# Kernel tuning notes

Hardware: AMD Instinct MI355X
Metric: run time of the kernel (lower is better)

## Reference

```python
import jax, jax.numpy as jnp
import numpy as np

EMBED_DIM = 1024
NUM_HEADS = 16
HEAD_DIM = EMBED_DIM // NUM_HEADS


def setup_inputs() -> dict:
    key = jax.random.key(0)
    ks = jax.random.split(key, 9)
    B, S, E = 2, 2048, EMBED_DIM
    scale = 1.0 / np.sqrt(E)
    inp = {
        "x": jax.random.normal(ks[0], (B, S, E), dtype=jnp.float32),
        "Wq": jax.random.normal(ks[1], (E, E), dtype=jnp.float32) * scale,
        "bq": jnp.zeros((E,), dtype=jnp.float32),
        "Wk": jax.random.normal(ks[2], (E, E), dtype=jnp.float32) * scale,
        "bk": jnp.zeros((E,), dtype=jnp.float32),
        "Wv": jax.random.normal(ks[3], (E, E), dtype=jnp.float32) * scale,
        "bv": jnp.zeros((E,), dtype=jnp.float32),
        "Wo": jax.random.normal(ks[4], (E, E), dtype=jnp.float32) * scale,
        "bo": jnp.zeros((E,), dtype=jnp.float32),
    }
    return inp


def reference(x, Wq, bq, Wk, bk, Wv, bv, Wo, bo):
    B, S, E = x.shape
    H, D = NUM_HEADS, HEAD_DIM
    sm_scale = D ** (-0.5)

    def proj(W, b):
        # torch Linear: x @ W.T + b ; reshape to [B, H, S, D]
        y = jnp.einsum("bse,fe->bsf", x, W) + b
        return y.reshape(B, S, H, D).transpose(0, 2, 1, 3)

    q = proj(Wq, bq)  # [B, H, S, D]
    k = proj(Wk, bk)
    v = proj(Wv, bv)

    scores = jnp.einsum("bhqd,bhkd->bhqk", q, k) * sm_scale  # [B, H, S, S]
    attn = jax.nn.softmax(scores, axis=-1)
    o = jnp.einsum("bhqk,bhkd->bhqd", attn, v)  # [B, H, S, D]
    o = o.transpose(0, 2, 1, 3).reshape(B, S, E)
    return jnp.einsum("bse,fe->bsf", o, Wo) + bo
```

## Files before the change

### kernel.cpp

```cpp
#include <hip/hip_runtime.h>
#include <hip/hip_fp16.h>
#include <stdint.h>


typedef _Float16 f16;
typedef _Float16 f16x8 __attribute__((ext_vector_type(8)));
typedef _Float16 f16x4v __attribute__((ext_vector_type(4)));
typedef float f32x4 __attribute__((ext_vector_type(4)));
typedef int i32x4 __attribute__((ext_vector_type(4)));

#define BQ  2
#define SEQ 2048
#define EMB 1024
#define NH  16
#define HD  64
#define MM  (BQ * SEQ)

__device__ __forceinline__ void gld_lds16(const void* g, void* l) {
  __builtin_amdgcn_global_load_lds(
      (const __attribute__((address_space(1))) void*)g,
      (__attribute__((address_space(3))) void*)l, 16, 0, 0);
}

__device__ __forceinline__ void stage128x64(const f16* __restrict__ src,
                                            int ld, f16* lds, int tid) {
#pragma unroll
  for (int it = 0; it < 4; ++it) {
    int idx = it * 256 + tid;
    int r = idx >> 3, c = idx & 7;
    int sc = c ^ (r & 7);
    gld_lds16(src + (size_t)r * ld + sc * 8, lds + idx * 8);
  }
}

__device__ __forceinline__ f16x8 pack8(float a0, float a1, float a2, float a3,
                                       float b0, float b1, float b2, float b3) {
  i32x4 w;
  w.x = __builtin_bit_cast(int, __builtin_amdgcn_cvt_pkrtz(a0, a1));
  w.y = __builtin_bit_cast(int, __builtin_amdgcn_cvt_pkrtz(a2, a3));
  w.z = __builtin_bit_cast(int, __builtin_amdgcn_cvt_pkrtz(b0, b1));
  w.w = __builtin_bit_cast(int, __builtin_amdgcn_cvt_pkrtz(b2, b3));
  return __builtin_bit_cast(f16x8, w);
}

__global__ void cvt4(const float* __restrict__ src, f16* __restrict__ dst,
                     int n4) {
  int i = blockIdx.x * blockDim.x + threadIdx.x;
  if (i < n4) {
    float4 v = ((const float4*)src)[i];
    f16x4v o;
    o[0] = (f16)v.x; o[1] = (f16)v.y; o[2] = (f16)v.z; o[3] = (f16)v.w;
    ((f16x4v*)dst)[i] = o;
  }
}

__global__ void cvtW4(const float* __restrict__ s0, const float* __restrict__ s1,
                      const float* __restrict__ s2, const float* __restrict__ s3,
                      f16* __restrict__ d0, f16* __restrict__ d1,
                      f16* __restrict__ d2, f16* __restrict__ d3, int n4) {
  int i = blockIdx.x * blockDim.x + threadIdx.x;
  if (i >= n4) return;
  const float* s = (blockIdx.y == 0) ? s0 : (blockIdx.y == 1) ? s1
                   : (blockIdx.y == 2) ? s2 : s3;
  f16* d = (blockIdx.y == 0) ? d0 : (blockIdx.y == 1) ? d1
           : (blockIdx.y == 2) ? d2 : d3;
  float4 v = ((const float4*)s)[i];
  f16x4v o;
  o[0] = (f16)v.x; o[1] = (f16)v.y; o[2] = (f16)v.z; o[3] = (f16)v.w;
  ((f16x4v*)d)[i] = o;
}

template <int MODE>
__global__ __launch_bounds__(256, 2) void gemm_bt(
    const f16* __restrict__ A, const f16* __restrict__ W0,
    const f16* __restrict__ W1, const f16* __restrict__ W2,
    const float* __restrict__ b0, const float* __restrict__ b1,
    const float* __restrict__ b2, f16* __restrict__ o0, f16* __restrict__ o1,
    f16* __restrict__ o2, float* __restrict__ fo) {
  __shared__ __align__(16) f16 As[128 * 64];
  __shared__ __align__(16) f16 Bs[128 * 64];

  const int tid = threadIdx.x, lane = tid & 63, wid = tid >> 6;
  const int z = blockIdx.z;
  const f16* W = (z == 0) ? W0 : (z == 1 ? W1 : W2);
  const float* bia = (z == 0) ? b0 : (z == 1 ? b1 : b2);
  f16* outp = (z == 0) ? o0 : (z == 1 ? o1 : o2);
  const int row0 = blockIdx.x * 128, col0 = blockIdx.y * 128;
  const int wr = (wid >> 1) * 64, wc = (wid & 1) * 64;
  const int rb = lane & 15, gq = lane >> 4, sw = lane & 7;

  f32x4 acc[4][4] = {};

  for (int kt = 0; kt < EMB / 64; ++kt) {
    __syncthreads();
    stage128x64(A + (size_t)row0 * EMB + kt * 64, EMB, As, tid);
    stage128x64(W + (size_t)col0 * EMB + kt * 64, EMB, Bs, tid);
    asm volatile("s_waitcnt vmcnt(0)" ::: "memory");
    __syncthreads();
#pragma unroll
    for (int kk = 0; kk < 2; ++kk) {
      f16x8 av[4], bv[4];
#pragma unroll
      for (int f = 0; f < 4; ++f) {
        av[f] = *(const f16x8*)(As + (wr + f * 16 + rb) * 64 +
                                (((kk * 4 + gq) ^ sw) << 3));
        bv[f] = *(const f16x8*)(Bs + (wc + f * 16 + rb) * 64 +
                                (((kk * 4 + gq) ^ sw) << 3));
      }
#pragma unroll
      for (int fi = 0; fi < 4; ++fi)
#pragma unroll
        for (int fj = 0; fj < 4; ++fj)
          acc[fi][fj] = __builtin_amdgcn_mfma_f32_16x16x32_f16(
              av[fi], bv[fj], acc[fi][fj], 0, 0, 0);
    }
  }

  float bias[4];
#pragma unroll
  for (int fj = 0; fj < 4; ++fj) bias[fj] = bia[col0 + wc + fj * 16 + rb];
  const float scale = (MODE == 0 && z == 0) ? 0.18033688011112042f : 1.0f;
#pragma unroll
  for (int fi = 0; fi < 4; ++fi) {
#pragma unroll
    for (int i = 0; i < 4; ++i) {
      int row = row0 + wr + fi * 16 + gq * 4 + i;
#pragma unroll
      for (int fj = 0; fj < 4; ++fj) {
        int col = col0 + wc + fj * 16 + rb;
        float v = (acc[fi][fj][i] + bias[fj]) * scale;
        if (MODE == 0) {
          int bb = row >> 11, s = row & (SEQ - 1);
          int h = col >> 6, d = col & 63;
          outp[(((size_t)(bb * NH + h)) * SEQ + s) * HD + d] = (f16)v;
        } else {
          fo[(size_t)row * EMB + col] = v;
        }
      }
    }
  }
}

__global__ __launch_bounds__(256) void vtrans(const f16* __restrict__ V,
                                              f16* __restrict__ Vt) {
  __shared__ f16 T[64][72];
  const int tid = threadIdx.x;
  const int s0 = blockIdx.x * 64, bh = blockIdx.y;
  const f16* Vh = V + (size_t)bh * SEQ * HD;
  f16* Vth = Vt + (size_t)bh * HD * SEQ;
#pragma unroll
  for (int it = 0; it < 2; ++it) {
    int idx = it * 256 + tid;
    int r = idx >> 3, c0 = (idx & 7) * 8;
    *(f16x8*)&T[r][c0] = *(const f16x8*)(Vh + (size_t)(s0 + r) * HD + c0);
  }
  __syncthreads();
#pragma unroll
  for (int it = 0; it < 2; ++it) {
    int idx = it * 256 + tid;
    int d = idx >> 3, a = idx & 7;
    f16x8 v;
#pragma unroll
    for (int j = 0; j < 8; ++j) v[j] = T[a * 8 + j][d];
    const int base = ((a >> 2) << 5) + ((a & 1) << 4) + (((a >> 1) & 1) << 2);
    f16* dst = Vth + (size_t)d * SEQ + s0 + base;
    f16x4v w0, w1;
#pragma unroll
    for (int j = 0; j < 4; ++j) { w0[j] = v[j]; w1[j] = v[4 + j]; }
    *(f16x4v*)dst = w0;
    *(f16x4v*)(dst + 8) = w1;
  }
}

__global__ __launch_bounds__(256, 3) void attn_fwd(const f16* __restrict__ Q,
                                                   const f16* __restrict__ K,
                                                   const f16* __restrict__ Vt,
                                                   f16* __restrict__ O) {
  __shared__ __align__(16) f16 Ks[3][64 * 64];
  __shared__ __align__(16) f16 Vs[3][64 * 64];

  const int tid = threadIdx.x, lane = tid & 63;
  const int wid = tid >> 6;
  const int orig = blockIdx.x;
  const int swz = ((orig & 7) << 6) + (orig >> 3);
  const int qt = swz & 15, bh = swz >> 4;
  const f16* Qh = Q + (size_t)bh * SEQ * HD;
  const f16* Kh = K + (size_t)bh * SEQ * HD;
  const f16* Vth = Vt + (size_t)bh * HD * SEQ;
  const int q0 = qt * 128 + wid * 32;
  const int rb = lane & 15, gq = lane >> 4, sw = lane & 7;

  f16x8 aq[2][2];
#pragma unroll
  for (int qf = 0; qf < 2; ++qf)
#pragma unroll
    for (int kk = 0; kk < 2; ++kk)
      aq[qf][kk] = *(const f16x8*)(Qh + (size_t)(q0 + qf * 16 + rb) * HD +
                                   kk * 32 + gq * 8);
  asm volatile("s_waitcnt vmcnt(0)" ::: "memory");

  const int srow = tid >> 3, scol = (tid & 7) ^ (srow & 7);
  const f16* Kg0 = Kh + (size_t)srow * HD + scol * 8;
  const f16* Vg0 = Vth + (size_t)srow * SEQ + scol * 8;

  const int NT = SEQ / 64;
#pragma unroll
  for (int p = 0; p < 2; ++p) {
    const f16* kg = Kg0 + (size_t)p * 64 * HD;
    const f16* vg = Vg0 + p * 64;
    gld_lds16(kg,            &Ks[p][tid * 8]);
    gld_lds16(kg + 32 * HD,  &Ks[p][(tid + 256) * 8]);
    gld_lds16(vg,            &Vs[p][tid * 8]);
    gld_lds16(vg + 32 * SEQ, &Vs[p][(tid + 256) * 8]);
  }

  f32x4 oacc[2][4] = {};
  float lsum[2] = {0.f, 0.f};

  for (int t = 0; t < NT; ++t) {
    __builtin_amdgcn_s_barrier();
    __builtin_amdgcn_sched_barrier(0);
    {
      const int tp = (t + 2 < NT) ? t + 2 : NT - 1;
      f16* Kn = &Ks[(t + 2) % 3][0];
      f16* Vn = &Vs[(t + 2) % 3][0];
      const f16* kg = Kg0 + (size_t)tp * 64 * HD;
      const f16* vg = Vg0 + tp * 64;
      gld_lds16(kg,            Kn + tid * 8);
      gld_lds16(kg + 32 * HD,  Kn + (tid + 256) * 8);
      gld_lds16(vg,            Vn + tid * 8);
      gld_lds16(vg + 32 * SEQ, Vn + (tid + 256) * 8);
      asm volatile("s_waitcnt vmcnt(8)" ::: "memory");
    }
    __builtin_amdgcn_s_barrier();
    __builtin_amdgcn_sched_barrier(0);

    const f16* Kb = &Ks[t % 3][0];
    const f16* Vb = &Vs[t % 3][0];

    f32x4 s_[2][4] = {};
#pragma unroll
    for (int kk = 0; kk < 2; ++kk) {
      f16x8 bk[4];
#pragma unroll
      for (int cf = 0; cf < 4; ++cf)
        bk[cf] = *(const f16x8*)(Kb + (cf * 16 + rb) * 64 +
                                 (((kk * 4 + gq) ^ sw) << 3));
#pragma unroll
      for (int qf = 0; qf < 2; ++qf)
#pragma unroll
        for (int cf = 0; cf < 4; ++cf)
          s_[qf][cf] = __builtin_amdgcn_mfma_f32_16x16x32_f16(
              bk[cf], aq[qf][kk], s_[qf][cf], 0, 0, 0);
    }

    f16x8 bp[2][2];
#pragma unroll
    for (int qf = 0; qf < 2; ++qf)
#pragma unroll
      for (int g = 0; g < 2; ++g) {
        float e0 = __builtin_amdgcn_exp2f(s_[qf][2 * g][0]);
        float e1 = __builtin_amdgcn_exp2f(s_[qf][2 * g][1]);
        float e2 = __builtin_amdgcn_exp2f(s_[qf][2 * g][2]);
        float e3 = __builtin_amdgcn_exp2f(s_[qf][2 * g][3]);
        float f0 = __builtin_amdgcn_exp2f(s_[qf][2 * g + 1][0]);
        float f1 = __builtin_amdgcn_exp2f(s_[qf][2 * g + 1][1]);
        float f2 = __builtin_amdgcn_exp2f(s_[qf][2 * g + 1][2]);
        float f3 = __builtin_amdgcn_exp2f(s_[qf][2 * g + 1][3]);
        lsum[qf] += ((e0 + e1) + (e2 + e3)) + ((f0 + f1) + (f2 + f3));
        bp[qf][g] = pack8(e0, e1, e2, e3, f0, f1, f2, f3);
      }

#pragma unroll
    for (int g = 0; g < 2; ++g) {
#pragma unroll
      for (int df = 0; df < 4; ++df) {
        f16x8 vb = *(const f16x8*)(Vb + (df * 16 + rb) * 64 +
                                   (((g * 4 + gq) ^ sw) << 3));
        oacc[0][df] = __builtin_amdgcn_mfma_f32_16x16x32_f16(bp[0][g], vb,
                                                             oacc[0][df], 0, 0, 0);
        oacc[1][df] = __builtin_amdgcn_mfma_f32_16x16x32_f16(bp[1][g], vb,
                                                             oacc[1][df], 0, 0, 0);
      }
    }
  }
  asm volatile("s_waitcnt vmcnt(0)" ::: "memory");

  float lv[2];
#pragma unroll
  for (int qf = 0; qf < 2; ++qf) {
    float l = lsum[qf];
    l += __shfl_xor(l, 16, 64);
    l += __shfl_xor(l, 32, 64);
    lv[qf] = l;
  }

  const int b = bh >> 4, h = bh & 15;
#pragma unroll
  for (int qf = 0; qf < 2; ++qf)
#pragma unroll
    for (int i = 0; i < 4; ++i) {
      const int rsel = (gq * 4 + i) & 15;
      const float l = __shfl(lv[qf], (lane & 48) + rsel, 64);
      const float inv = 1.0f / l;
      const int s = q0 + qf * 16 + gq * 4 + i;
      f16* orow = O + ((size_t)(b * SEQ + s)) * EMB + h * 64 + rb;
#pragma unroll
      for (int df = 0; df < 4; ++df)
        orow[df * 16] = (f16)(oacc[qf][df][i] * inv);
    }
}

extern "C" void kernel_launch(void* const* d_in, const int* in_sizes, int n_in,
                              void* d_out, int out_size, void* d_ws,
                              size_t ws_size, hipStream_t stream) {
  const float* x = (const float*)d_in[0];
  const float* Wq = (const float*)d_in[1];
  const float* bq = (const float*)d_in[2];
  const float* Wk = (const float*)d_in[3];
  const float* bk = (const float*)d_in[4];
  const float* Wv = (const float*)d_in[5];
  const float* bv = (const float*)d_in[6];
  const float* Wo = (const float*)d_in[7];
  const float* bo = (const float*)d_in[8];
  float* out = (float*)d_out;

  const size_t NX = (size_t)MM * EMB;
  const size_t NW = (size_t)EMB * EMB;

  f16* xh  = (f16*)d_ws;
  f16* wqh = xh + NX;
  f16* wkh = wqh + NW;
  f16* wvh = wkh + NW;
  f16* woh = wvh + NW;
  f16* Qw  = woh + NW;
  f16* Kw  = Qw + NX;
  f16* Vw  = Kw + NX;
  f16* Vtw = Vw + NX;
  f16* Ow  = Vtw + NX;

  cvt4<<<(int)(NX / 4 / 256), 256, 0, stream>>>(x, xh, (int)(NX / 4));
  cvtW4<<<dim3((int)(NW / 4 / 256), 4), 256, 0, stream>>>(
      Wq, Wk, Wv, Wo, wqh, wkh, wvh, woh, (int)(NW / 4));

  gemm_bt<0><<<dim3(MM / 128, EMB / 128, 3), 256, 0, stream>>>(
      xh, wqh, wkh, wvh, bq, bk, bv, Qw, Kw, Vw, nullptr);

  vtrans<<<dim3(SEQ / 64, BQ * NH), 256, 0, stream>>>(Vw, Vtw);

  attn_fwd<<<dim3(512), 256, 0, stream>>>(Qw, Kw, Vtw, Ow);

  gemm_bt<1><<<dim3(MM / 128, EMB / 128, 1), 256, 0, stream>>>(
      Ow, woh, woh, woh, bo, bo, bo, nullptr, nullptr, nullptr, out);
}
```

Before: 109.2 us.

## Split attention block into 8 waves of 16 query rows each

The attention kernel moves from 4 waves each handling 32 query rows to 8 waves each handling 16 rows, launched with 512 threads per block. Each thread now stages one 16-byte chunk of K and V per tile instead of two, and the wait count is adjusted to match. The aim is more waves for latency hiding and lower register pressure per wave. In exchange, each K/V fragment read from LDS feeds only one query fragment instead of two, which doubles LDS read traffic per MFMA and adds barrier cost across more waves.

```diff
diff --git a/kernel.cpp b/kernel.cpp
--- a/kernel.cpp
+++ b/kernel.cpp
@@ -172,7 +172,7 @@
   }
 }
 
-__global__ __launch_bounds__(256, 3) void attn_fwd(const f16* __restrict__ Q,
+__global__ __launch_bounds__(512, 4) void attn_fwd(const f16* __restrict__ Q,
                                                    const f16* __restrict__ K,
                                                    const f16* __restrict__ Vt,
                                                    f16* __restrict__ O) {
@@ -187,16 +187,13 @@
   const f16* Qh = Q + (size_t)bh * SEQ * HD;
   const f16* Kh = K + (size_t)bh * SEQ * HD;
   const f16* Vth = Vt + (size_t)bh * HD * SEQ;
-  const int q0 = qt * 128 + wid * 32;
+  const int q0 = qt * 128 + wid * 16;
   const int rb = lane & 15, gq = lane >> 4, sw = lane & 7;
 
-  f16x8 aq[2][2];
-#pragma unroll
-  for (int qf = 0; qf < 2; ++qf)
-#pragma unroll
-    for (int kk = 0; kk < 2; ++kk)
-      aq[qf][kk] = *(const f16x8*)(Qh + (size_t)(q0 + qf * 16 + rb) * HD +
-                                   kk * 32 + gq * 8);
+  f16x8 aq[2];
+#pragma unroll
+  for (int kk = 0; kk < 2; ++kk)
+    aq[kk] = *(const f16x8*)(Qh + (size_t)(q0 + rb) * HD + kk * 32 + gq * 8);
   asm volatile("s_waitcnt vmcnt(0)" ::: "memory");
 
   const int srow = tid >> 3, scol = (tid & 7) ^ (srow & 7);
@@ -206,31 +203,21 @@
   const int NT = SEQ / 64;
 #pragma unroll
   for (int p = 0; p < 2; ++p) {
-    const f16* kg = Kg0 + (size_t)p * 64 * HD;
-    const f16* vg = Vg0 + p * 64;
-    gld_lds16(kg,            &Ks[p][tid * 8]);
-    gld_lds16(kg + 32 * HD,  &Ks[p][(tid + 256) * 8]);
-    gld_lds16(vg,            &Vs[p][tid * 8]);
-    gld_lds16(vg + 32 * SEQ, &Vs[p][(tid + 256) * 8]);
-  }
-
-  f32x4 oacc[2][4] = {};
-  float lsum[2] = {0.f, 0.f};
+    gld_lds16(Kg0 + (size_t)p * 64 * HD, &Ks[p][tid * 8]);
+    gld_lds16(Vg0 + p * 64,              &Vs[p][tid * 8]);
+  }
+
+  f32x4 oacc[4] = {};
+  float lsum = 0.f;
 
   for (int t = 0; t < NT; ++t) {
     __builtin_amdgcn_s_barrier();
     __builtin_amdgcn_sched_barrier(0);
     {
       const int tp = (t + 2 < NT) ? t + 2 : NT - 1;
-      f16* Kn = &Ks[(t + 2) % 3][0];
-      f16* Vn = &Vs[(t + 2) % 3][0];
-      const f16* kg = Kg0 + (size_t)tp * 64 * HD;
-      const f16* vg = Vg0 + tp * 64;
-      gld_lds16(kg,            Kn + tid * 8);
-      gld_lds16(kg + 32 * HD,  Kn + (tid + 256) * 8);
-      gld_lds16(vg,            Vn + tid * 8);
-      gld_lds16(vg + 32 * SEQ, Vn + (tid + 256) * 8);
-      asm volatile("s_waitcnt vmcnt(8)" ::: "memory");
+      gld_lds16(Kg0 + (size_t)tp * 64 * HD, &Ks[(t + 2) % 3][tid * 8]);
+      gld_lds16(Vg0 + tp * 64,              &Vs[(t + 2) % 3][tid * 8]);
+      asm volatile("s_waitcnt vmcnt(4)" ::: "memory");
     }
     __builtin_amdgcn_s_barrier();
     __builtin_amdgcn_sched_barrier(0);
@@ -238,7 +225,7 @@
     const f16* Kb = &Ks[t % 3][0];
     const f16* Vb = &Vs[t % 3][0];
 
-    f32x4 s_[2][4] = {};
+    f32x4 s_[4] = {};
 #pragma unroll
     for (int kk = 0; kk < 2; ++kk) {
       f16x8 bk[4];
@@ -247,68 +234,54 @@
         bk[cf] = *(const f16x8*)(Kb + (cf * 16 + rb) * 64 +
                                  (((kk * 4 + gq) ^ sw) << 3));
 #pragma unroll
-      for (int qf = 0; qf < 2; ++qf)
-#pragma unroll
-        for (int cf = 0; cf < 4; ++cf)
-          s_[qf][cf] = __builtin_amdgcn_mfma_f32_16x16x32_f16(
-              bk[cf], aq[qf][kk], s_[qf][cf], 0, 0, 0);
-    }
-
-    f16x8 bp[2][2];
-#pragma unroll
-    for (int qf = 0; qf < 2; ++qf)
-#pragma unroll
-      for (int g = 0; g < 2; ++g) {
-        float e0 = __builtin_amdgcn_exp2f(s_[qf][2 * g][0]);
-        float e1 = __builtin_amdgcn_exp2f(s_[qf][2 * g][1]);
-        float e2 = __builtin_amdgcn_exp2f(s_[qf][2 * g][2]);
-        float e3 = __builtin_amdgcn_exp2f(s_[qf][2 * g][3]);
-        float f0 = __builtin_amdgcn_exp2f(s_[qf][2 * g + 1][0]);
-        float f1 = __builtin_amdgcn_exp2f(s_[qf][2 * g + 1][1]);
-        float f2 = __builtin_amdgcn_exp2f(s_[qf][2 * g + 1][2]);
-        float f3 = __builtin_amdgcn_exp2f(s_[qf][2 * g + 1][3]);
-        lsum[qf] += ((e0 + e1) + (e2 + e3)) + ((f0 + f1) + (f2 + f3));
-        bp[qf][g] = pack8(e0, e1, e2, e3, f0, f1, f2, f3);
-      }
-
+      for (int cf = 0; cf < 4; ++cf)
+        s_[cf] = __builtin_amdgcn_mfma_f32_16x16x32_f16(bk[cf], aq[kk],
+                                                        s_[cf], 0, 0, 0);
+    }
+
+    f16x8 bp[2];
 #pragma unroll
     for (int g = 0; g < 2; ++g) {
+      float e0 = __builtin_amdgcn_exp2f(s_[2 * g][0]);
+      float e1 = __builtin_amdgcn_exp2f(s_[2 * g][1]);
+      float e2 = __builtin_amdgcn_exp2f(s_[2 * g][2]);
+      float e3 = __builtin_amdgcn_exp2f(s_[2 * g][3]);
+      float f0 = __builtin_amdgcn_exp2f(s_[2 * g + 1][0]);
+      float f1 = __builtin_amdgcn_exp2f(s_[2 * g + 1][1]);
+      float f2 = __builtin_amdgcn_exp2f(s_[2 * g + 1][2]);
+      float f3 = __builtin_amdgcn_exp2f(s_[2 * g + 1][3]);
+      lsum += ((e0 + e1) + (e2 + e3)) + ((f0 + f1) + (f2 + f3));
+      bp[g] = pack8(e0, e1, e2, e3, f0, f1, f2, f3);
+    }
+
+#pragma unroll
+    for (int g = 0; g < 2; ++g)
 #pragma unroll
       for (int df = 0; df < 4; ++df) {
         f16x8 vb = *(const f16x8*)(Vb + (df * 16 + rb) * 64 +
                                    (((g * 4 + gq) ^ sw) << 3));
-        oacc[0][df] = __builtin_amdgcn_mfma_f32_16x16x32_f16(bp[0][g], vb,
-                                                             oacc[0][df], 0, 0, 0);
-        oacc[1][df] = __builtin_amdgcn_mfma_f32_16x16x32_f16(bp[1][g], vb,
-                                                             oacc[1][df], 0, 0, 0);
+        oacc[df] = __builtin_amdgcn_mfma_f32_16x16x32_f16(bp[g], vb,
+                                                          oacc[df], 0, 0, 0);
       }
-    }
   }
   asm volatile("s_waitcnt vmcnt(0)" ::: "memory");
 
-  float lv[2];
-#pragma unroll
-  for (int qf = 0; qf < 2; ++qf) {
-    float l = lsum[qf];
-    l += __shfl_xor(l, 16, 64);
-    l += __shfl_xor(l, 32, 64);
-    lv[qf] = l;
-  }
+  float lv = lsum;
+  lv += __shfl_xor(lv, 16, 64);
+  lv += __shfl_xor(lv, 32, 64);
 
   const int b = bh >> 4, h = bh & 15;
 #pragma unroll
-  for (int qf = 0; qf < 2; ++qf)
-#pragma unroll
-    for (int i = 0; i < 4; ++i) {
-      const int rsel = (gq * 4 + i) & 15;
-      const float l = __shfl(lv[qf], (lane & 48) + rsel, 64);
-      const float inv = 1.0f / l;
-      const int s = q0 + qf * 16 + gq * 4 + i;
-      f16* orow = O + ((size_t)(b * SEQ + s)) * EMB + h * 64 + rb;
-#pragma unroll
-      for (int df = 0; df < 4; ++df)
-        orow[df * 16] = (f16)(oacc[qf][df][i] * inv);
-    }
+  for (int i = 0; i < 4; ++i) {
+    const int rsel = (gq * 4 + i) & 15;
+    const float l = __shfl(lv, (lane & 48) + rsel, 64);
+    const float inv = 1.0f / l;
+    const int s = q0 + gq * 4 + i;
+    f16* orow = O + ((size_t)(b * SEQ + s)) * EMB + h * 64 + rb;
+#pragma unroll
+    for (int df = 0; df < 4; ++df)
+      orow[df * 16] = (f16)(oacc[df][i] * inv);
+  }
 }
 
 extern "C" void kernel_launch(void* const* d_in, const int* in_sizes, int n_in,
@@ -348,7 +321,7 @@
 
   vtrans<<<dim3(SEQ / 64, BQ * NH), 256, 0, stream>>>(Vw, Vtw);
 
-  attn_fwd<<<dim3(512), 256, 0, stream>>>(Qw, Kw, Vtw, Ow);
+  attn_fwd<<<dim3(512), 512, 0, stream>>>(Qw, Kw, Vtw, Ow);
 
   gemm_bt<1><<<dim3(MM / 128, EMB / 128, 1), 256, 0, stream>>>(
       Ow, woh, woh, woh, bo, bo, bo, nullptr, nullptr, nullptr, out);
```

Result: no change. 111.1 us (+1.8%).
